# Performance work log

Hardware: AMD Instinct MI355X
Metric: run time of the kernel (lower is better)

The kernel has to match this reference:

```python
import jax, jax.numpy as jnp
import numpy as np

OBS, ACT, HID, P, B = 128, 32, 256, 64, 4096
EPS = 1e-5


def _block(x, W, b, g, be, act=True):
    # x: [B, P, Din]; W: [P, Din, Dout]; b/g/be: [P, Dout]
    y = jnp.einsum('bpi,pio->bpo', x, W) + b
    # GroupNorm with one group per sub-policy: normalize over Dout per (b, p)
    mu = jnp.mean(y, axis=-1, keepdims=True)
    var = jnp.var(y, axis=-1, keepdims=True)
    y = (y - mu) * jax.lax.rsqrt(var + EPS) * g + be
    return jax.nn.elu(y) if act else y


def setup_inputs() -> dict:
    key = jax.random.key(0)
    ks = jax.random.split(key, 17)
    s = 0.05
    return {
        'observation': jax.random.normal(ks[0], (B, OBS), dtype=jnp.float32),
        'W1': jax.random.normal(ks[1], (P, OBS, HID), dtype=jnp.float32) * s,
        'b1': jax.random.normal(ks[2], (P, HID), dtype=jnp.float32) * s,
        'g1': jnp.ones((P, HID), dtype=jnp.float32),
        'be1': jnp.zeros((P, HID), dtype=jnp.float32),
        'W2': jax.random.normal(ks[3], (P, HID, HID), dtype=jnp.float32) * s,
        'b2': jax.random.normal(ks[4], (P, HID), dtype=jnp.float32) * s,
        'g2': jnp.ones((P, HID), dtype=jnp.float32),
        'be2': jnp.zeros((P, HID), dtype=jnp.float32),
        'W3': jax.random.normal(ks[5], (P, HID, HID), dtype=jnp.float32) * s,
        'b3': jax.random.normal(ks[6], (P, HID), dtype=jnp.float32) * s,
        'g3': jnp.ones((P, HID), dtype=jnp.float32),
        'be3': jnp.zeros((P, HID), dtype=jnp.float32),
        'W4': jax.random.normal(ks[7], (P, HID, ACT), dtype=jnp.float32) * s,
        'b4': jax.random.normal(ks[8], (P, ACT), dtype=jnp.float32) * s,
        'g4': jnp.ones((P, ACT), dtype=jnp.float32),
        'be4': jnp.zeros((P, ACT), dtype=jnp.float32),
    }


def reference(observation, W1, b1, g1, be1, W2, b2, g2, be2,
              W3, b3, g3, be3, W4, b4, g4, be4):
    # broadcast observation to each sub-policy: [B, P, OBS]
    x = jnp.broadcast_to(observation[:, None, :], (observation.shape[0], P, OBS))
    x = _block(x, W1, b1, g1, be1, act=True)
    x = _block(x, W2, b2, g2, be2, act=True)
    x = _block(x, W3, b3, g3, be3, act=True)
    x = _block(x, W4, b4, g4, be4, act=False)
    return x  # [B, P, ACT] action logits
```

## Files before the change

### kernel.cpp

```cpp
#include <hip/hip_runtime.h>

#define B_    4096
#define P_    64
#define OBS_  128
#define HID_  256
#define ACTD_ 32

typedef __attribute__((ext_vector_type(8)))  __bf16 bf16x8;
typedef __attribute__((ext_vector_type(4)))  float  f32x4;
typedef __attribute__((ext_vector_type(16))) float  f32x16;

#define XSTRIDE 264

#define WS1 0L
#define WS2 2097152L
#define WS3 6291456L
#define WS4 10485760L

__device__ __forceinline__ unsigned short f2bf(float x) {
    unsigned u = __builtin_bit_cast(unsigned, x);
    u = (u + 0x7fffu + ((u >> 16) & 1u)) >> 16;
    return (unsigned short)u;
}

__device__ __forceinline__ float elu_asm(float v) {
    float r;
    asm volatile(
        "v_mul_f32 %0, 0x3fb8aa3b, %1\n\t"
        "v_exp_f32 %0, %0\n\t"
        "s_nop 1\n\t"
        "v_add_f32 %0, -1.0, %0\n\t"
        "v_cmp_lt_f32 vcc, 0, %1\n\t"
        "v_cndmask_b32 %0, %0, %1, vcc"
        : "=&v"(r) : "v"(v) : "vcc");
    return r;
}

template<int K, int N>
__device__ __forceinline__ void prep_body(const float* __restrict__ W,
                                          unsigned short* __restrict__ out,
                                          int b, int t)
{
    constexpr int CH = K / 32;
    int tid  = b * 256 + t;
    int n    = tid % N;
    int rest = tid / N;
    int u    = rest % 4;
    rest    /= 4;
    int c    = rest % CH;
    int p    = rest / CH;
    const float* src = W + ((long)(p * K + c * 32 + u * 8)) * N + n;
    unsigned short tmp[8];
#pragma unroll
    for (int j = 0; j < 8; ++j) tmp[j] = f2bf(src[(long)j * N]);
    unsigned short* dst = out + ((((long)(p * CH + c) * 4 + u) * N + n) * 8);
    *reinterpret_cast<uint4*>(dst) = *reinterpret_cast<const uint4*>(tmp);
}

extern "C" __global__ __launch_bounds__(256)
void prep_all(const float* __restrict__ W1, const float* __restrict__ W2,
              const float* __restrict__ W3, const float* __restrict__ W4,
              unsigned short* __restrict__ ws)
{
    int b = blockIdx.x, t = threadIdx.x;
    if      (b < 1024) prep_body<128, 256>(W1, ws + WS1, b,        t);
    else if (b < 3072) prep_body<256, 256>(W2, ws + WS2, b - 1024, t);
    else if (b < 5120) prep_body<256, 256>(W3, ws + WS3, b - 3072, t);
    else               prep_body<256, 32 >(W4, ws + WS4, b - 5120, t);
}

__device__ __forceinline__ void stage(char* lds, const char* src, int nbytes, int tid)
{
    const int lnoff = (tid & 63) * 16;
    const int off   = (tid >> 6) * 1024 + lnoff;
    for (int i = off; i < nbytes; i += 4096) {
        __builtin_amdgcn_global_load_lds(
            (const __attribute__((address_space(1))) unsigned int*)(const void*)(src + i),
            (__attribute__((address_space(3))) unsigned int*)(void*)(lds + (i - lnoff)),
            16, 0, 0);
    }
}

template<int KCH>
__device__ __forceinline__ void layer256(
    unsigned short* __restrict__ X,
    char* __restrict__ Wb0, char* __restrict__ Wb1,
    const char* __restrict__ wsrc,
    const char* __restrict__ nsrc, int nbytes,
    const float* __restrict__ bp, const float* __restrict__ gp, const float* __restrict__ bep,
    float2* __restrict__ part, float2* __restrict__ stats,
    int tid, bool elu)
{
    const int w  = tid >> 6;
    const int l5 = tid & 31;
    const int h  = (tid & 63) >> 5;

    f32x16 acc[2][2];
#pragma unroll
    for (int rt = 0; rt < 2; ++rt)
#pragma unroll
        for (int ct = 0; ct < 2; ++ct)
#pragma unroll
            for (int r = 0; r < 16; ++r) acc[rt][ct][r] = 0.f;

    for (int c = 0; c < KCH; ++c) {
        const char* nx = (c + 1 < KCH) ? (wsrc + (long)(c + 1) * 8192) : nsrc;
        int nb         = (c + 1 < KCH) ? 8192 : nbytes;
        stage((c & 1) ? Wb0 : Wb1, nx, nb, tid);

        const char* wc = (c & 1) ? Wb1 : Wb0;
        const int k0 = c * 16 + h * 8;
        bf16x8 a0 = *(const bf16x8*)(X + l5 * XSTRIDE + k0);
        bf16x8 a1 = *(const bf16x8*)(X + (32 + l5) * XSTRIDE + k0);
        const char* bb = wc + h * 4096;
        bf16x8 b0 = *(const bf16x8*)(bb + (w * 64 + l5) * 16);
        bf16x8 b1 = *(const bf16x8*)(bb + (w * 64 + 32 + l5) * 16);
        acc[0][0] = __builtin_amdgcn_mfma_f32_32x32x16_bf16(a0, b0, acc[0][0], 0, 0, 0);
        acc[1][0] = __builtin_amdgcn_mfma_f32_32x32x16_bf16(a1, b0, acc[1][0], 0, 0, 0);
        acc[0][1] = __builtin_amdgcn_mfma_f32_32x32x16_bf16(a0, b1, acc[0][1], 0, 0, 0);
        acc[1][1] = __builtin_amdgcn_mfma_f32_32x32x16_bf16(a1, b1, acc[1][1], 0, 0, 0);
        __syncthreads();
    }

    const int n0 = w * 64 + l5, n1 = n0 + 32;
    const float bb0 = bp[n0], bb1 = bp[n1];
#pragma unroll
    for (int rt = 0; rt < 2; ++rt)
#pragma unroll
        for (int r = 0; r < 16; ++r) { acc[rt][0][r] += bb0; acc[rt][1][r] += bb1; }

#pragma unroll
    for (int rt = 0; rt < 2; ++rt)
#pragma unroll
        for (int r = 0; r < 16; ++r) {
            const int row = rt * 32 + (r & 3) + 8 * (r >> 2) + 4 * h;
            X[row * XSTRIDE + n0] = f2bf(acc[rt][0][r]);
            X[row * XSTRIDE + n1] = f2bf(acc[rt][1][r]);
        }
    __syncthreads();

    {
        const int lane = tid & 63;
        float s = 0.f, s2 = 0.f;
#pragma unroll
        for (int j8 = 0; j8 < 8; ++j8) {
            bf16x8 v8 = *(const bf16x8*)(X + lane * XSTRIDE + w * 64 + j8 * 8);
#pragma unroll
            for (int e = 0; e < 8; ++e) { float v = (float)v8[e]; s += v; s2 = fmaf(v, v, s2); }
        }
        part[lane * 4 + w] = make_float2(s, s2);
    }
    __syncthreads();
    if (w == 0) {
        const int lane = tid & 63;
        float2 p0 = part[lane * 4 + 0], p1 = part[lane * 4 + 1];
        float2 p2 = part[lane * 4 + 2], p3 = part[lane * 4 + 3];
        float s  = p0.x + p1.x + p2.x + p3.x;
        float s2 = p0.y + p1.y + p2.y + p3.y;
        float mu  = s * (1.f / 256.f);
        float var = s2 * (1.f / 256.f) - mu * mu;
        stats[lane] = make_float2(mu, rsqrtf(var + 1e-5f));
    }
    __syncthreads();

    const float g0 = gp[n0], g1 = gp[n1], be0 = bep[n0], be1 = bep[n1];
#pragma unroll
    for (int rt = 0; rt < 2; ++rt)
#pragma unroll
        for (int r = 0; r < 16; ++r) {
            const int row = rt * 32 + (r & 3) + 8 * (r >> 2) + 4 * h;
            float2 st = stats[row];
            float v0 = (acc[rt][0][r] - st.x) * st.y * g0 + be0;
            float v1 = (acc[rt][1][r] - st.x) * st.y * g1 + be1;
            if (elu) { v0 = elu_asm(v0); v1 = elu_asm(v1); }
            X[row * XSTRIDE + n0] = f2bf(v0);
            X[row * XSTRIDE + n1] = f2bf(v1);
        }
    __syncthreads();
}

__device__ __forceinline__ void layer32(
    const unsigned short* __restrict__ X,
    char* __restrict__ Wb0, char* __restrict__ Wb1,
    const char* __restrict__ wsrc,
    const float* __restrict__ bp, const float* __restrict__ gp, const float* __restrict__ bep,
    float* __restrict__ outg, int bbase, int p, int tid)
{
    const int w = tid >> 6, lane = tid & 63, ln = lane & 15, quad = lane >> 4;
    f32x4 acc[2];
#pragma unroll
    for (int nt = 0; nt < 2; ++nt)
#pragma unroll
        for (int r = 0; r < 4; ++r) acc[nt][r] = 0.f;

    for (int c = 0; c < 8; ++c) {
        if (c < 7) stage((c & 1) ? Wb0 : Wb1, wsrc + (long)(c + 1) * 2048, 2048, tid);
        const char* wc = (c & 1) ? Wb1 : Wb0;
        bf16x8 a  = *(const bf16x8*)(X + (16 * w + ln) * XSTRIDE + c * 32 + quad * 8);
        bf16x8 b0 = *(const bf16x8*)(wc + quad * 512 + ln * 16);
        bf16x8 b1 = *(const bf16x8*)(wc + quad * 512 + (16 + ln) * 16);
        acc[0] = __builtin_amdgcn_mfma_f32_16x16x32_bf16(a, b0, acc[0], 0, 0, 0);
        acc[1] = __builtin_amdgcn_mfma_f32_16x16x32_bf16(a, b1, acc[1], 0, 0, 0);
        __syncthreads();
    }

    const float bb0 = bp[ln], bb1 = bp[16 + ln];
    const float g0 = gp[ln], g1 = gp[16 + ln], be0 = bep[ln], be1 = bep[16 + ln];
#pragma unroll
    for (int r = 0; r < 4; ++r) {
        float y0 = acc[0][r] + bb0, y1 = acc[1][r] + bb1;
        float s = y0 + y1, s2 = y0 * y0 + y1 * y1;
        s += __shfl_xor(s, 1);  s2 += __shfl_xor(s2, 1);
        s += __shfl_xor(s, 2);  s2 += __shfl_xor(s2, 2);
        s += __shfl_xor(s, 4);  s2 += __shfl_xor(s2, 4);
        s += __shfl_xor(s, 8);  s2 += __shfl_xor(s2, 8);
        float mu  = s * (1.f / 32.f);
        float var = s2 * (1.f / 32.f) - mu * mu;
        float rs  = rsqrtf(var + 1e-5f);
        const int row = bbase + 16 * w + quad * 4 + r;
        float* o = outg + ((long)row * P_ + p) * ACTD_;
        o[ln]      = (y0 - mu) * rs * g0 + be0;
        o[16 + ln] = (y1 - mu) * rs * g1 + be1;
    }
}

extern "C" __global__ void __launch_bounds__(256, 3)
policy_fused(const float* __restrict__ obs,
             const unsigned short* __restrict__ wbf,
             const float* __restrict__ b1, const float* __restrict__ g1, const float* __restrict__ be1,
             const float* __restrict__ b2, const float* __restrict__ g2, const float* __restrict__ be2,
             const float* __restrict__ b3, const float* __restrict__ g3, const float* __restrict__ be3,
             const float* __restrict__ b4, const float* __restrict__ g4, const float* __restrict__ be4,
             float* __restrict__ out)
{
    __shared__ __align__(16) unsigned short X[64 * XSTRIDE];
    __shared__ __align__(16) char Wbuf0[8192];
    __shared__ __align__(16) char Wbuf1[8192];
    __shared__ float2 part[64 * 4];
    __shared__ float2 stats[64];

    const int tid = threadIdx.x;
    const int bx  = blockIdx.x;
    const int p     = ((bx & 7) << 3) | ((bx >> 3) & 7);
    const int bbase = (bx >> 6) * 64;

    const char* ws1 = (const char*)(wbf + WS1 + (long)p * (128 * 256));
    const char* ws2 = (const char*)(wbf + WS2 + (long)p * (256 * 256));
    const char* ws3 = (const char*)(wbf + WS3 + (long)p * (256 * 256));
    const char* ws4 = (const char*)(wbf + WS4 + (long)p * (256 * 32));

    stage(Wbuf0, ws1, 8192, tid);

    for (int idx = tid; idx < 64 * 32; idx += 256) {
        int row = idx >> 5, c4 = idx & 31;
        float4 v = *reinterpret_cast<const float4*>(obs + (long)(bbase + row) * OBS_ + c4 * 4);
        uint2 pk;
        pk.x = (unsigned)f2bf(v.x) | ((unsigned)f2bf(v.y) << 16);
        pk.y = (unsigned)f2bf(v.z) | ((unsigned)f2bf(v.w) << 16);
        *reinterpret_cast<uint2*>(X + row * XSTRIDE + c4 * 4) = pk;
    }
    __syncthreads();

    layer256<8>(X, Wbuf0, Wbuf1, ws1, ws2, 8192,
                b1 + p * 256, g1 + p * 256, be1 + p * 256, part, stats, tid, true);
    layer256<16>(X, Wbuf0, Wbuf1, ws2, ws3, 8192,
                 b2 + p * 256, g2 + p * 256, be2 + p * 256, part, stats, tid, true);
    layer256<16>(X, Wbuf0, Wbuf1, ws3, ws4, 2048,
                 b3 + p * 256, g3 + p * 256, be3 + p * 256, part, stats, tid, true);
    layer32(X, Wbuf0, Wbuf1, ws4,
            b4 + p * 32, g4 + p * 32, be4 + p * 32, out, bbase, p, tid);
}

extern "C" void kernel_launch(void* const* d_in, const int* in_sizes, int n_in,
                              void* d_out, int out_size, void* d_ws, size_t ws_size,
                              hipStream_t stream)
{
    const float* obs = (const float*)d_in[0];
    const float* W1  = (const float*)d_in[1];
    const float* b1  = (const float*)d_in[2];
    const float* g1  = (const float*)d_in[3];
    const float* be1 = (const float*)d_in[4];
    const float* W2  = (const float*)d_in[5];
    const float* b2  = (const float*)d_in[6];
    const float* g2  = (const float*)d_in[7];
    const float* be2 = (const float*)d_in[8];
    const float* W3  = (const float*)d_in[9];
    const float* b3  = (const float*)d_in[10];
    const float* g3  = (const float*)d_in[11];
    const float* be3 = (const float*)d_in[12];
    const float* W4  = (const float*)d_in[13];
    const float* b4  = (const float*)d_in[14];
    const float* g4  = (const float*)d_in[15];
    const float* be4 = (const float*)d_in[16];
    float* out = (float*)d_out;
    unsigned short* ws = (unsigned short*)d_ws;

    hipLaunchKernelGGL(prep_all, dim3(5376), dim3(256), 0, stream, W1, W2, W3, W4, ws);

    hipLaunchKernelGGL(policy_fused, dim3(4096), dim3(256), 0, stream,
                       obs, ws,
                       b1, g1, be1, b2, g2, be2, b3, g3, be3, b4, g4, be4, out);
}
```

Before: 322.8 us.

## Interleave activation columns in LDS and permute weight K order to match

Each lane now writes its two output columns (n0, n0+32) as one packed 32-bit bf16 pair at adjacent LDS positions instead of two separate 16-bit stores. To keep the math correct, the prep kernel permutes the K ordering of W2, W3 and W4 so that the weight rows line up with the interleaved activation layout. This halves the number of LDS stores in the epilogue, at the cost of a more complex, strided gather in the weight prep kernel. The per-row statistics are unaffected because the row sums do not depend on column order.

```diff
diff --git a/kernel.cpp b/kernel.cpp
--- a/kernel.cpp
+++ b/kernel.cpp
@@ -21,6 +21,14 @@
     unsigned u = __builtin_bit_cast(unsigned, x);
     u = (u + 0x7fffu + ((u >> 16) & 1u)) >> 16;
     return (unsigned short)u;
+}
+
+__device__ __forceinline__ unsigned pack_bf16_rne(float a, float b) {
+    unsigned ua = __builtin_bit_cast(unsigned, a);
+    unsigned ub = __builtin_bit_cast(unsigned, b);
+    ua = ua + 0x7fffu + ((ua >> 16) & 1u);
+    ub = ub + 0x7fffu + ((ub >> 16) & 1u);
+    return __builtin_amdgcn_perm(ub, ua, 0x07060302u);
 }
 
 __device__ __forceinline__ float elu_asm(float v) {
@@ -36,7 +44,7 @@
     return r;
 }
 
-template<int K, int N>
+template<int K, int N, bool PERM>
 __device__ __forceinline__ void prep_body(const float* __restrict__ W,
                                           unsigned short* __restrict__ out,
                                           int b, int t)
@@ -49,10 +57,13 @@
     rest    /= 4;
     int c    = rest % CH;
     int p    = rest / CH;
-    const float* src = W + ((long)(p * K + c * 32 + u * 8)) * N + n;
     unsigned short tmp[8];
 #pragma unroll
-    for (int j = 0; j < 8; ++j) tmp[j] = f2bf(src[(long)j * N]);
+    for (int j = 0; j < 8; ++j) {
+        int sk = c * 32 + u * 8 + j;
+        int k  = PERM ? ((sk & ~63) | ((sk & 1) << 5) | ((sk >> 1) & 31)) : sk;
+        tmp[j] = f2bf(W[((long)(p * K + k)) * N + n]);
+    }
     unsigned short* dst = out + ((((long)(p * CH + c) * 4 + u) * N + n) * 8);
     *reinterpret_cast<uint4*>(dst) = *reinterpret_cast<const uint4*>(tmp);
 }
@@ -63,10 +74,10 @@
               unsigned short* __restrict__ ws)
 {
     int b = blockIdx.x, t = threadIdx.x;
-    if      (b < 1024) prep_body<128, 256>(W1, ws + WS1, b,        t);
-    else if (b < 3072) prep_body<256, 256>(W2, ws + WS2, b - 1024, t);
-    else if (b < 5120) prep_body<256, 256>(W3, ws + WS3, b - 3072, t);
-    else               prep_body<256, 32 >(W4, ws + WS4, b - 5120, t);
+    if      (b < 1024) prep_body<128, 256, false>(W1, ws + WS1, b,        t);
+    else if (b < 3072) prep_body<256, 256, true >(W2, ws + WS2, b - 1024, t);
+    else if (b < 5120) prep_body<256, 256, true >(W3, ws + WS3, b - 3072, t);
+    else               prep_body<256, 32,  true >(W4, ws + WS4, b - 5120, t);
 }
 
 __device__ __forceinline__ void stage(char* lds, const char* src, int nbytes, int tid)
@@ -123,6 +134,7 @@
     }
 
     const int n0 = w * 64 + l5, n1 = n0 + 32;
+    const int pos = w * 64 + 2 * l5;
     const float bb0 = bp[n0], bb1 = bp[n1];
 #pragma unroll
     for (int rt = 0; rt < 2; ++rt)
@@ -134,8 +146,8 @@
 #pragma unroll
         for (int r = 0; r < 16; ++r) {
             const int row = rt * 32 + (r & 3) + 8 * (r >> 2) + 4 * h;
-            X[row * XSTRIDE + n0] = f2bf(acc[rt][0][r]);
-            X[row * XSTRIDE + n1] = f2bf(acc[rt][1][r]);
+            *reinterpret_cast<unsigned*>(X + row * XSTRIDE + pos) =
+                pack_bf16_rne(acc[rt][0][r], acc[rt][1][r]);
         }
     __syncthreads();
 
@@ -173,8 +185,7 @@
             float v0 = (acc[rt][0][r] - st.x) * st.y * g0 + be0;
             float v1 = (acc[rt][1][r] - st.x) * st.y * g1 + be1;
             if (elu) { v0 = elu_asm(v0); v1 = elu_asm(v1); }
-            X[row * XSTRIDE + n0] = f2bf(v0);
-            X[row * XSTRIDE + n1] = f2bf(v1);
+            *reinterpret_cast<unsigned*>(X + row * XSTRIDE + pos) = pack_bf16_rne(v0, v1);
         }
     __syncthreads();
 }
```

Result: faster. 308.1 us (-4.6%).
